# Kernel optimization log

Measured on AMD Instinct MI355X. Metric: run time of the kernel, lower is better.

Reference implementation:

```python
import jax, jax.numpy as jnp
import numpy as np

DIM = 256
NUM_HEADS = 8
HEAD_DIM = DIM // NUM_HEADS
Z_SHAPE = (32, 32)   # template grid -> qL = 1024
X_SHAPE = (64, 64)   # search grid  -> kvL = 4096
TBL = (max(Z_SHAPE[0], X_SHAPE[0]), max(Z_SHAPE[1], X_SHAPE[1]))  # (64, 64)
N_TABLE = (2 * TBL[0] - 1) * (2 * TBL[1] - 1)  # 16129


def _make_rel_index():
    """Faithful replication of the torch module's buffer construction (numpy, vectorized)."""
    H, W = TBL
    coords = np.stack(np.meshgrid(np.arange(H), np.arange(W), indexing='ij'), 0).reshape(2, -1)
    rel = coords[:, :, None] - coords[:, None, :]                     # (2, HW, HW)
    idx = (rel[0] + H - 1) * (2 * W - 1) + (rel[1] + W - 1)           # (HW, HW)
    h_z_begin = int(H / 2 - Z_SHAPE[0] / 2); h_x_begin = int(H / 2 - X_SHAPE[0] / 2)
    w_z_begin = int(W / 2 - Z_SHAPE[1] / 2); w_x_begin = int(W / 2 - X_SHAPE[1] / 2)
    hz = np.arange(h_z_begin, h_z_begin + Z_SHAPE[0])
    hx = np.arange(h_x_begin, h_x_begin + X_SHAPE[0])
    wz = np.arange(w_z_begin, w_z_begin + Z_SHAPE[1])
    wx = np.arange(w_x_begin, w_x_begin + X_SHAPE[1])
    # NOTE: source multiplies by z_2d_shape[0]/z_2d_shape[1] (kept faithfully, even though it looks odd)
    z_pos = hz[:, None] * Z_SHAPE[0] + wz[None, :]                    # (32, 32) axes (h_z, w_z)
    x_pos = hx[:, None] * Z_SHAPE[1] + wx[None, :]                    # (64, 64) axes (h_x, w_x)
    g = idx[z_pos][:, :, x_pos]                                       # (h_z, w_z, h_x, w_x)
    g = g.transpose(0, 2, 1, 3).reshape(Z_SHAPE[0] * Z_SHAPE[1], X_SHAPE[0] * X_SHAPE[1])
    return jnp.asarray(g, dtype=jnp.int32)                           # (qL, kvL)


def setup_inputs() -> dict:
    key = jax.random.key(0)
    ks = jax.random.split(key, 10)
    B, qL, kvL, C = 4, Z_SHAPE[0] * Z_SHAPE[1], X_SHAPE[0] * X_SHAPE[1], DIM
    return {
        'q': jax.random.normal(ks[0], (B, qL, C), jnp.float32),
        'kv': jax.random.normal(ks[1], (B, kvL, C), jnp.float32),
        'Wq': jax.random.normal(ks[2], (C, C), jnp.float32) * 0.02,
        'bq': jnp.zeros((C,), jnp.float32),
        'Wkv': jax.random.normal(ks[3], (2 * C, C), jnp.float32) * 0.02,
        'bkv': jnp.zeros((2 * C,), jnp.float32),
        'bias_table': jax.random.normal(ks[4], (N_TABLE, NUM_HEADS), jnp.float32) * 0.02,
        'Wp': jax.random.normal(ks[5], (C, C), jnp.float32) * 0.02,
        'bp': jnp.zeros((C,), jnp.float32),
        'rel_index': _make_rel_index(),
    }


def reference(q, kv, Wq, bq, Wkv, bkv, bias_table, Wp, bp, rel_index):
    B, qL, C = q.shape
    kvL = kv.shape[1]
    H, hd = NUM_HEADS, HEAD_DIM
    scale = hd ** (-0.5)
    Q = (q @ Wq.T + bq).reshape(B, qL, H, hd) * scale                  # bqhd
    KV = (kv @ Wkv.T + bkv).reshape(B, kvL, 2, H, hd)
    K, V = KV[:, :, 0], KV[:, :, 1]                                    # bkhd
    attn = jnp.einsum('bqhd,bkhd->bhqk', Q, K)                         # (B,H,qL,kvL)
    bias = bias_table[rel_index]                                       # (qL,kvL,H)
    attn = attn + jnp.transpose(bias, (2, 0, 1))[None]
    attn = jax.nn.softmax(attn, axis=-1)
    x = jnp.einsum('bhqk,bkhd->bqhd', attn, V).reshape(B, qL, C)
    return x @ Wp.T + bp
```

## Files before the change

### kernel.cpp

```cpp
#include <hip/hip_runtime.h>
#include <math.h>

#define DIM 256
#define NUM_HEADS 8
#define HEAD_DIM 32
#define QL 1024
#define KVL 4096
#define BATCH 4
#define NTAB 16129
#define LOG2E 1.4426950408889634f

typedef __attribute__((ext_vector_type(8))) short short8;
typedef __attribute__((ext_vector_type(4))) float floatx4;
typedef __attribute__((ext_vector_type(4))) unsigned short ushort4v;

__device__ inline unsigned short f2bf(float x) {
    unsigned u = __builtin_bit_cast(unsigned, x);
    unsigned r = (u + 0x7FFFu + ((u >> 16) & 1u)) >> 16;
    return (unsigned short)r;
}
__device__ inline float bf2f(unsigned short h) {
    return __builtin_bit_cast(float, (unsigned)h << 16);
}
__device__ inline floatx4 mfma16(short8 a, short8 b, floatx4 c) {
    return __builtin_amdgcn_mfma_f32_16x16x32_bf16(a, b, c, 0, 0, 0);
}

__global__ __launch_bounds__(256) void split_all(
    const float* __restrict__ q, const float* __restrict__ kv,
    const float* __restrict__ Wq, const float* __restrict__ Wkv,
    const float* __restrict__ Wp, const float* __restrict__ bias_table,
    unsigned short* __restrict__ qh, unsigned short* __restrict__ kvh,
    unsigned short* __restrict__ Wqh, unsigned short* __restrict__ Wkvh,
    unsigned short* __restrict__ Wph, unsigned short* __restrict__ Wpl,
    float* __restrict__ Bt)
{
    const int gid = blockIdx.x * 256 + threadIdx.x;
    if (gid >= 1408514) return;
    if (gid >= 1376256) {
        const int local = gid - 1376256;
        const float4 v = ((const float4*)bias_table)[local];
        const float vv[4] = {v.x, v.y, v.z, v.w};
        const int base = local * 4;
#pragma unroll
        for (int j = 0; j < 4; ++j) {
            const int i = (base + j) >> 3, h = (base + j) & 7;
            Bt[h * NTAB + i] = vv[j] * LOG2E;
        }
        return;
    }
    const float* src; unsigned short* dh; unsigned short* dl = nullptr; int local;
    if (gid < 262144)       { src = q;   dh = qh;   local = gid; }
    else if (gid < 1310720) { src = kv;  dh = kvh;  local = gid - 262144; }
    else if (gid < 1327104) { src = Wq;  dh = Wqh;  local = gid - 1310720; }
    else if (gid < 1359872) { src = Wkv; dh = Wkvh; local = gid - 1327104; }
    else                    { src = Wp;  dh = Wph;  dl = Wpl; local = gid - 1359872; }
    const float4 v = ((const float4*)src)[local];
    ushort4v h;
    h[0] = f2bf(v.x); h[1] = f2bf(v.y); h[2] = f2bf(v.z); h[3] = f2bf(v.w);
    ((ushort4v*)dh)[local] = h;
    if (dl) {
        ushort4v l;
        l[0] = f2bf(v.x - bf2f(h[0])); l[1] = f2bf(v.y - bf2f(h[1]));
        l[2] = f2bf(v.z - bf2f(h[2])); l[3] = f2bf(v.w - bf2f(h[3]));
        ((ushort4v*)dl)[local] = l;
    }
}

template<int MODE, int BW>
__global__ __launch_bounds__(BW * 64) void gemm_bf16(
    const unsigned short* __restrict__ Ah, const unsigned short* __restrict__ Al,
    const unsigned short* __restrict__ Wh, const unsigned short* __restrict__ Wl,
    const float* __restrict__ bias, float* __restrict__ Cf,
    unsigned short* __restrict__ Cb, float scale)
{
    constexpr bool THREE = (MODE == 0);
    const int t    = threadIdx.x;
    const int w    = t >> 6;
    const int lane = t & 63;
    const int n16  = lane & 15;
    const int quad = lane >> 4;
    const int m0 = blockIdx.y * (BW * 32) + w * 32;
    const int n0 = blockIdx.x * 64;

    floatx4 acc[2][4];
#pragma unroll
    for (int s = 0; s < 2; ++s)
#pragma unroll
        for (int c = 0; c < 4; ++c) acc[s][c] = (floatx4){0.f, 0.f, 0.f, 0.f};

    short8 af[2][2], afl[2][2], wf[2][4], wfl[2][4];

    auto LD = [&](int kb, int bi) {
#pragma unroll
        for (int s = 0; s < 2; ++s) {
            af[bi][s] = *(const short8*)(Ah + (size_t)(m0 + s * 16 + n16) * 256 + kb + quad * 8);
            if (THREE)
                afl[bi][s] = *(const short8*)(Al + (size_t)(m0 + s * 16 + n16) * 256 + kb + quad * 8);
        }
#pragma unroll
        for (int c = 0; c < 4; ++c) {
            wf[bi][c] = *(const short8*)(Wh + (size_t)(n0 + c * 16 + n16) * 256 + kb + quad * 8);
            if (THREE)
                wfl[bi][c] = *(const short8*)(Wl + (size_t)(n0 + c * 16 + n16) * 256 + kb + quad * 8);
        }
    };

    LD(0, 0);
#pragma unroll
    for (int i = 0; i < 8; ++i) {
        const int cur = i & 1, nxt = cur ^ 1;
        if (i < 7) LD((i + 1) * 32, nxt);
#pragma unroll
        for (int c = 0; c < 4; ++c)
#pragma unroll
            for (int s = 0; s < 2; ++s) {
                acc[s][c] = mfma16(af[cur][s], wf[cur][c], acc[s][c]);
                if (THREE) {
                    acc[s][c] = mfma16(af[cur][s], wfl[cur][c], acc[s][c]);
                    acc[s][c] = mfma16(afl[cur][s], wf[cur][c], acc[s][c]);
                }
            }
    }

#pragma unroll
    for (int s = 0; s < 2; ++s)
#pragma unroll
        for (int c = 0; c < 4; ++c) {
            const floatx4 v = acc[s][c];
            const int n_g = n0 + c * 16 + n16;
#pragma unroll
            for (int r = 0; r < 4; ++r) {
                const int m_g = m0 + s * 16 + quad * 4 + r;
                const float val = v[r];
                if (MODE == 0) {
                    Cf[(size_t)m_g * 256 + n_g] = val + bias[n_g];
                } else if (MODE == 1) {
                    const int h = n_g >> 5, d = n_g & 31;
                    const int b = m_g >> 10, qq = m_g & 1023;
                    Cb[(((size_t)(b * 8 + h) * 1024 + qq) << 5) + d] =
                        f2bf((val + bias[n_g]) * scale);
                } else if (MODE == 2) {
                    const int h = n_g >> 5, d = n_g & 31;
                    const int b = m_g >> 12, kvr = m_g & 4095;
                    Cb[(((size_t)(b * 8 + h) * 4096 + kvr) << 5) + d] =
                        f2bf(val + bias[n_g]);
                } else {
                    const int h = m_g >> 5, dd = m_g & 31;
                    const int b = n_g >> 12, kvr = n_g & 4095;
                    Cb[(((size_t)((b * 8 + h) * 32 + dd)) << 12) + kvr] =
                        f2bf(val + bias[m_g]);
                }
            }
        }
}

__global__ __launch_bounds__(256, 3) void attn_mfma(
    const unsigned short* __restrict__ Qb,
    const unsigned short* __restrict__ Kb,
    const unsigned short* __restrict__ Vt,
    const float* __restrict__ Bt,
    float* __restrict__ Op,
    float* __restrict__ lp)
{
    const int qt = blockIdx.x;
    const int h  = blockIdx.y;
    const int b  = blockIdx.z >> 2;
    const int sp = blockIdx.z & 3;
    const int bh = b * NUM_HEADS + h;
    const int tid  = threadIdx.x;
    const int w    = tid >> 6;
    const int lane = tid & 63;
    const int n    = lane & 15;
    const int quad = lane >> 4;

    __shared__ __align__(16) unsigned short Ps[4][16 * 72];

    const int qrowA = qt * 64 + w * 16 + n;
    const short8 qf = *(const short8*)(Qb + (((size_t)bh * QL + qrowA) << 5) + quad * 8);

    const int qgC = qt * 64 + w * 16 + quad * 4;
    const float* Bth = Bt + h * NTAB;

    const int vS = sp >> 1;
    int ivals[4];
    int M[4][4];
#pragma unroll
    for (int r = 0; r < 4; ++r) {
        const int q = qgC + r;
        ivals[r] = q >> 5;
        const int B0 = (((q & 31) << 1) + vS) << 5;
#pragma unroll
        for (int c = 0; c < 4; ++c) {
            const int bb = B0 + c * 16 + n;
            M[r][c] = (bb >> 6) * 127 + (bb & 63);
        }
    }

    floatx4 o0 = {0.f, 0.f, 0.f, 0.f};
    floatx4 o1 = {0.f, 0.f, 0.f, 0.f};
    float lacc[4] = {0.f, 0.f, 0.f, 0.f};

    const unsigned short* Kbase = Kb + (((size_t)bh * KVL) << 5);
    const unsigned short* Vbase = Vt + (((size_t)bh * 32) << 12);
    const int kbase = sp * 1024;

    short8 kf[2][4];
    auto LDK = [&](int kt, int bi) {
        const int kv0 = kbase + kt * 64;
#pragma unroll
        for (int c = 0; c < 4; ++c)
            kf[bi][c] = *(const short8*)(Kbase + ((size_t)(kv0 + c * 16 + n) << 5) + quad * 8);
    };

    LDK(0, 0);

#pragma unroll
    for (int kt = 0; kt < 16; ++kt) {
        const int cur = kt & 1, nxt = cur ^ 1;
        const int kv0 = kbase + kt * 64;

        const int jS = ((sp << 4) + kt) & 31;
        float bv[16];
#pragma unroll
        for (int r = 0; r < 4; ++r) {
            const int a  = 528 + (ivals[r] << 5) + jS;
            const int A0 = ((a >> 6) + 63) * 127 + (a & 63) + 63;
#pragma unroll
            for (int c = 0; c < 4; ++c)
                bv[r * 4 + c] = Bth[A0 - M[r][c]];
        }

        short8 vf[2][2];
#pragma unroll
        for (int kc = 0; kc < 2; ++kc)
#pragma unroll
            for (int dh = 0; dh < 2; ++dh)
                vf[kc][dh] = *(const short8*)(Vbase + ((size_t)(dh * 16 + n) << 12)
                                              + kv0 + kc * 32 + quad * 8);

        if (kt < 15) LDK(kt + 1, nxt);

        floatx4 sc[4];
#pragma unroll
        for (int c = 0; c < 4; ++c) {
            floatx4 z = {0.f, 0.f, 0.f, 0.f};
            sc[c] = mfma16(qf, kf[cur][c], z);
        }

#pragma unroll
        for (int r = 0; r < 4; ++r)
#pragma unroll
            for (int c = 0; c < 4; ++c) {
                const float p = exp2f(fmaf(sc[c][r], LOG2E, bv[r * 4 + c]));
                lacc[r] += p;
                Ps[w][(quad * 4 + r) * 72 + c * 16 + n] = f2bf(p);
            }
        asm volatile("s_waitcnt lgkmcnt(0)" ::: "memory");

#pragma unroll
        for (int kc = 0; kc < 2; ++kc) {
            const short8 pf = *(const short8*)(Ps[w] + n * 72 + kc * 32 + quad * 8);
            o0 = mfma16(pf, vf[kc][0], o0);
            o1 = mfma16(pf, vf[kc][1], o1);
        }
        asm volatile("" ::: "memory");
    }

#pragma unroll
    for (int r = 0; r < 4; ++r) {
        float v = lacc[r];
        v += __shfl_xor(v, 1, 16);
        v += __shfl_xor(v, 2, 16);
        v += __shfl_xor(v, 4, 16);
        v += __shfl_xor(v, 8, 16);
        lacc[r] = v;
    }

    float* Opb = Op + (((size_t)(sp * 32 + bh) * QL) << 5);
#pragma unroll
    for (int r = 0; r < 4; ++r) {
        const int qg = qgC + r;
        Opb[((size_t)qg << 5) + n]      = o0[r];
        Opb[((size_t)qg << 5) + 16 + n] = o1[r];
    }
    if (n == 0) {
        float* lpb = lp + (size_t)(sp * 32 + bh) * QL;
#pragma unroll
        for (int r = 0; r < 4; ++r) lpb[qgC + r] = lacc[r];
    }
}

__global__ __launch_bounds__(256) void attn_combine(
    const float* __restrict__ Op, const float* __restrict__ lp,
    unsigned short* __restrict__ Xh, unsigned short* __restrict__ Xl)
{
    const int gid = blockIdx.x * 256 + threadIdx.x;
    const int bhq = gid >> 5, d = gid & 31;
    const int bh = bhq >> 10, q = bhq & 1023;
    const int b = bh >> 3, hh = bh & 7;
    float o = 0.f, l = 0.f;
#pragma unroll
    for (int s = 0; s < 4; ++s) {
        o += Op[((size_t)(s * 32768 + bhq) << 5) + d];
        l += lp[s * 32768 + bhq];
    }
    const float val = o / l;
    const size_t idx = ((size_t)(b * QL + q)) * DIM + hh * HEAD_DIM + d;
    const unsigned short h = f2bf(val);
    Xh[idx] = h;
    Xl[idx] = f2bf(val - bf2f(h));
}

extern "C" void kernel_launch(void* const* d_in, const int* in_sizes, int n_in,
                              void* d_out, int out_size, void* d_ws, size_t ws_size,
                              hipStream_t stream)
{
    const float* q          = (const float*)d_in[0];
    const float* kv         = (const float*)d_in[1];
    const float* Wq         = (const float*)d_in[2];
    const float* bq         = (const float*)d_in[3];
    const float* Wkv        = (const float*)d_in[4];
    const float* bkv        = (const float*)d_in[5];
    const float* bias_table = (const float*)d_in[6];
    const float* Wp         = (const float*)d_in[7];
    const float* bp         = (const float*)d_in[8];
    float* out = (float*)d_out;

    char* ws = (char*)d_ws;
    unsigned short* Qb   = (unsigned short*)(ws);
    unsigned short* Kb   = (unsigned short*)(ws + (size_t)(2u  << 20));
    unsigned short* Vt   = (unsigned short*)(ws + (size_t)(10u << 20));
    unsigned short* kvh  = (unsigned short*)(ws + (size_t)(18u << 20));
    float*          Op   = (float*)         (ws + (size_t)(18u << 20));
    float*          lp   = (float*)         (ws + (size_t)(34u << 20));
    float*          Bt   = (float*)         (ws + (size_t)(34u << 20) + (512u << 10));
    unsigned short* qh   = (unsigned short*)(ws + (size_t)(36u << 20));
    unsigned short* Wqh  = (unsigned short*)(ws + (size_t)(38u << 20));
    unsigned short* Wkvh = (unsigned short*)(ws + (size_t)(38u << 20) + (128u << 10));
    unsigned short* Wph  = (unsigned short*)(ws + (size_t)(38u << 20) + (384u << 10));
    unsigned short* Wpl  = (unsigned short*)(ws + (size_t)(38u << 20) + (512u << 10));
    unsigned short* Xh   = qh;
    unsigned short* Xl   = Vt;

    const float scale = 1.0f / sqrtf((float)HEAD_DIM);

    split_all<<<dim3(5503), 256, 0, stream>>>(q, kv, Wq, Wkv, Wp, bias_table,
                                              qh, kvh, Wqh, Wkvh, Wph, Wpl, Bt);
    gemm_bf16<1, 2><<<dim3(4, 64), 128, 0, stream>>>(
        qh, nullptr, Wqh, nullptr, bq, nullptr, Qb, scale);
    gemm_bf16<2, 4><<<dim3(4, 128), 256, 0, stream>>>(
        kvh, nullptr, Wkvh, nullptr, bkv, nullptr, Kb, 1.0f);
    gemm_bf16<3, 4><<<dim3(256, 2), 256, 0, stream>>>(
        Wkvh + 256 * 256, nullptr, kvh, nullptr, bkv + 256, nullptr, Vt, 1.0f);
    attn_mfma<<<dim3(16, 8, 16), 256, 0, stream>>>(Qb, Kb, Vt, Bt, Op, lp);
    attn_combine<<<dim3(4096), 256, 0, stream>>>(Op, lp, Xh, Xl);
    gemm_bf16<0, 2><<<dim3(4, 64), 128, 0, stream>>>(
        Xh, Xl, Wph, Wpl, bp, out, nullptr, 1.0f);
}
```

Measured before the change: 249.2 us.

## Fuse QKV projection GEMMs into one launch and prefetch bias gather in attention

```diff
diff --git a/kernel.cpp b/kernel.cpp
--- a/kernel.cpp
+++ b/kernel.cpp
@@ -68,11 +68,11 @@
 }
 
 template<int MODE, int BW>
-__global__ __launch_bounds__(BW * 64) void gemm_bf16(
+__device__ __forceinline__ void gemm_core(
     const unsigned short* __restrict__ Ah, const unsigned short* __restrict__ Al,
     const unsigned short* __restrict__ Wh, const unsigned short* __restrict__ Wl,
     const float* __restrict__ bias, float* __restrict__ Cf,
-    unsigned short* __restrict__ Cb, float scale)
+    unsigned short* __restrict__ Cb, float scale, int bx, int by)
 {
     constexpr bool THREE = (MODE == 0);
     const int t    = threadIdx.x;
@@ -80,8 +80,8 @@
     const int lane = t & 63;
     const int n16  = lane & 15;
     const int quad = lane >> 4;
-    const int m0 = blockIdx.y * (BW * 32) + w * 32;
-    const int n0 = blockIdx.x * 64;
+    const int m0 = by * (BW * 32) + w * 32;
+    const int n0 = bx * 64;
 
     floatx4 acc[2][4];
 #pragma unroll
@@ -155,6 +155,37 @@
         }
 }
 
+__global__ __launch_bounds__(256) void gemm_qkv(
+    const unsigned short* __restrict__ qh, const unsigned short* __restrict__ kvh,
+    const unsigned short* __restrict__ Wqh, const unsigned short* __restrict__ Wkvh,
+    const float* __restrict__ bq, const float* __restrict__ bkv,
+    unsigned short* __restrict__ Qb, unsigned short* __restrict__ Kb,
+    unsigned short* __restrict__ Vt, float scale)
+{
+    const int id = blockIdx.x;
+    if (id < 128) {
+        gemm_core<1, 4>(qh, nullptr, Wqh, nullptr, bq, nullptr, Qb, scale,
+                        id & 3, id >> 2);
+    } else if (id < 640) {
+        const int t2 = id - 128;
+        gemm_core<2, 4>(kvh, nullptr, Wkvh, nullptr, bkv, nullptr, Kb, 1.0f,
+                        t2 & 3, t2 >> 2);
+    } else {
+        const int t2 = id - 640;
+        gemm_core<3, 4>(Wkvh + 256 * 256, nullptr, kvh, nullptr, bkv + 256,
+                        nullptr, Vt, 1.0f, t2 >> 1, t2 & 1);
+    }
+}
+
+__global__ __launch_bounds__(128) void gemm_out(
+    const unsigned short* __restrict__ Xh, const unsigned short* __restrict__ Xl,
+    const unsigned short* __restrict__ Wph, const unsigned short* __restrict__ Wpl,
+    const float* __restrict__ bp, float* __restrict__ out)
+{
+    gemm_core<0, 2>(Xh, Xl, Wph, Wpl, bp, out, nullptr, 1.0f,
+                    blockIdx.x, blockIdx.y);
+}
+
 __global__ __launch_bounds__(256, 3) void attn_mfma(
     const unsigned short* __restrict__ Qb,
     const unsigned short* __restrict__ Kb,
@@ -163,10 +194,12 @@
     float* __restrict__ Op,
     float* __restrict__ lp)
 {
-    const int qt = blockIdx.x;
-    const int h  = blockIdx.y;
-    const int b  = blockIdx.z >> 2;
-    const int sp = blockIdx.z & 3;
+    const int id   = blockIdx.x;
+    const int qt   = id >> 7;
+    const int rest = id & 127;
+    const int h    = rest & 7;
+    const int sp   = (rest >> 3) & 3;
+    const int b    = rest >> 5;
     const int bh = b * NUM_HEADS + h;
     const int tid  = threadIdx.x;
     const int w    = tid >> 6;
@@ -206,31 +239,34 @@
     const int kbase = sp * 1024;
 
     short8 kf[2][4];
+    float  bv[2][16];
+
     auto LDK = [&](int kt, int bi) {
         const int kv0 = kbase + kt * 64;
 #pragma unroll
         for (int c = 0; c < 4; ++c)
             kf[bi][c] = *(const short8*)(Kbase + ((size_t)(kv0 + c * 16 + n) << 5) + quad * 8);
     };
+    auto GATHER = [&](int kt, int bi) {
+        const int jS = ((sp << 4) + kt) & 31;
+#pragma unroll
+        for (int r = 0; r < 4; ++r) {
+            const int a  = 528 + (ivals[r] << 5) + jS;
+            const int A0 = ((a >> 6) + 63) * 127 + (a & 63) + 63;
+#pragma unroll
+            for (int c = 0; c < 4; ++c)
+                bv[bi][r * 4 + c] = Bth[A0 - M[r][c]];
+        }
+    };
 
     LDK(0, 0);
-
-#pragma unroll
+    GATHER(0, 0);
+
+#pragma unroll 2
     for (int kt = 0; kt < 16; ++kt) {
         const int cur = kt & 1, nxt = cur ^ 1;
         const int kv0 = kbase + kt * 64;
 
-        const int jS = ((sp << 4) + kt) & 31;
-        float bv[16];
-#pragma unroll
-        for (int r = 0; r < 4; ++r) {
-            const int a  = 528 + (ivals[r] << 5) + jS;
-            const int A0 = ((a >> 6) + 63) * 127 + (a & 63) + 63;
-#pragma unroll
-            for (int c = 0; c < 4; ++c)
-                bv[r * 4 + c] = Bth[A0 - M[r][c]];
-        }
-
         short8 vf[2][2];
 #pragma unroll
         for (int kc = 0; kc < 2; ++kc)
@@ -239,8 +275,6 @@
                 vf[kc][dh] = *(const short8*)(Vbase + ((size_t)(dh * 16 + n) << 12)
                                               + kv0 + kc * 32 + quad * 8);
 
-        if (kt < 15) LDK(kt + 1, nxt);
-
         floatx4 sc[4];
 #pragma unroll
         for (int c = 0; c < 4; ++c) {
@@ -248,11 +282,13 @@
             sc[c] = mfma16(qf, kf[cur][c], z);
         }
 
+        if (kt < 15) { LDK(kt + 1, nxt); GATHER(kt + 1, nxt); }
+
 #pragma unroll
         for (int r = 0; r < 4; ++r)
 #pragma unroll
             for (int c = 0; c < 4; ++c) {
-                const float p = exp2f(fmaf(sc[c][r], LOG2E, bv[r * 4 + c]));
+                const float p = exp2f(fmaf(sc[c][r], LOG2E, bv[cur][r * 4 + c]));
                 lacc[r] += p;
                 Ps[w][(quad * 4 + r) * 72 + c * 16 + n] = f2bf(p);
             }
@@ -347,14 +383,9 @@
 
     split_all<<<dim3(5503), 256, 0, stream>>>(q, kv, Wq, Wkv, Wp, bias_table,
                                               qh, kvh, Wqh, Wkvh, Wph, Wpl, Bt);
-    gemm_bf16<1, 2><<<dim3(4, 64), 128, 0, stream>>>(
-        qh, nullptr, Wqh, nullptr, bq, nullptr, Qb, scale);
-    gemm_bf16<2, 4><<<dim3(4, 128), 256, 0, stream>>>(
-        kvh, nullptr, Wkvh, nullptr, bkv, nullptr, Kb, 1.0f);
-    gemm_bf16<3, 4><<<dim3(256, 2), 256, 0, stream>>>(
-        Wkvh + 256 * 256, nullptr, kvh, nullptr, bkv + 256, nullptr, Vt, 1.0f);
-    attn_mfma<<<dim3(16, 8, 16), 256, 0, stream>>>(Qb, Kb, Vt, Bt, Op, lp);
+    gemm_qkv<<<dim3(1152), 256, 0, stream>>>(qh, kvh, Wqh, Wkvh, bq, bkv,
+                                             Qb, Kb, Vt, scale);
+    attn_mfma<<<dim3(2048), 256, 0, stream>>>(Qb, Kb, Vt, Bt, Op, lp);
     attn_combine<<<dim3(4096), 256, 0, stream>>>(Op, lp, Xh, Xl);
-    gemm_bf16<0, 2><<<dim3(4, 64), 128, 0, stream>>>(
-        Xh, Xl, Wph, Wpl, bp, out, nullptr, 1.0f);
-}
+    gemm_out<<<dim3(4, 64), 128, 0, stream>>>(Xh, Xl, Wph, Wpl, bp, out);
+}
```

Result: slower. 372.5 us (+49.5%).
